# Performance work log

Hardware: AMD Instinct MI355X
Metric: run time of the kernel (lower is better)

## Reference

```python
import jax, jax.numpy as jnp
import numpy as np
import math

B, S, D, H = 2, 2048, 1024, 16
HD = D // H
KL_GAMMA = 0.1
EPS = 1e-10


def setup_inputs() -> dict:
    key = jax.random.key(0)
    ks = jax.random.split(key, 12)
    # positive inputs + positive weights keep scores > 0 so log(mean(scores)) is finite
    query = jax.random.uniform(ks[0], (B, S, D), dtype=jnp.float32)
    k_in = jax.random.uniform(ks[1], (B, S, D), dtype=jnp.float32)
    v_in = jax.random.uniform(ks[2], (B, S, D), dtype=jnp.float32)
    def w(k):
        return jax.random.uniform(k, (D, D), dtype=jnp.float32) * 0.002
    b = jnp.full((D,), 1e-3, dtype=jnp.float32)
    return {
        "query": query, "key": k_in, "value": v_in,
        "Wq": w(ks[3]), "bq": b,
        "Wk": w(ks[4]), "bk": b,
        "Wv": w(ks[5]), "bv": b,
        "Wo": w(ks[6]), "bo": b,
    }


def reference(query, key, value, Wq, bq, Wk, bk, Wv, bv, Wo, bo):
    Bq, Sq, _ = query.shape
    Sk = key.shape[1]
    # projections, split heads: [B, H, S, HD]
    Q = (query @ Wq + bq).reshape(Bq, Sq, H, HD).transpose(0, 2, 1, 3)
    K = (key @ Wk + bk).reshape(Bq, Sk, H, HD).transpose(0, 2, 1, 3)
    V = (value @ Wv + bv).reshape(Bq, Sk, H, HD).transpose(0, 2, 1, 3)
    scores = jnp.einsum("bhqd,bhkd->bhqk", Q, K) / math.sqrt(HD)  # [B,H,Sq,Sk]
    # KL bias: row-mean broadcast over keys, then log
    target = jnp.mean(scores, axis=-1, keepdims=True)  # [B,H,Sq,1]
    scores = scores + KL_GAMMA * jnp.log(target + EPS)
    attn = jax.nn.softmax(scores, axis=-1)
    ctx = jnp.einsum("bhqk,bhkd->bhqd", attn, V)
    ctx = ctx.transpose(0, 2, 1, 3).reshape(Bq, Sq, D)
    return ctx @ Wo + bo
```

## Files before the change

### kernel.cpp

```cpp
#include <hip/hip_runtime.h>
#include <hip/hip_bf16.h>
#include <stdint.h>


#define NB 2
#define NS 2048
#define ND 1024
#define NH 16
#define HD 64

typedef short bf16x8 __attribute__((ext_vector_type(8)));
typedef short bf16x4 __attribute__((ext_vector_type(4)));
typedef float f32x4 __attribute__((ext_vector_type(4)));
typedef float f32x16 __attribute__((ext_vector_type(16)));
typedef unsigned int u32x4 __attribute__((ext_vector_type(4)));

static __device__ __forceinline__ short f2bf(float f) {
    uint32_t u = __builtin_bit_cast(uint32_t, f);
    uint32_t r = (u + 0x7fffu + ((u >> 16) & 1u)) >> 16;
    return (short)(uint16_t)r;
}

static __device__ __forceinline__ unsigned int cvtpk(float lo, float hi) {
    unsigned int r;
    asm("v_cvt_pk_bf16_f32 %0, %1, %2" : "=v"(r) : "v"(lo), "v"(hi));
    return r;
}

#if __has_builtin(__builtin_amdgcn_exp2f)
#define EXP2(x) __builtin_amdgcn_exp2f(x)
#else
#define EXP2(x) exp2f(x)
#endif

static __device__ __forceinline__ void plswap(unsigned& a, unsigned& b) {
#if __has_builtin(__builtin_amdgcn_permlane32_swap)
    auto r = __builtin_amdgcn_permlane32_swap(a, b, false, false);
    a = r[0]; b = r[1];
#else
    const int l = (int)(threadIdx.x & 63);
    unsigned bl = __shfl(b, l & 31);
    unsigned ah = __shfl(a, (l & 31) + 32);
    a = (l < 32) ? a : bl;
    b = (l < 32) ? ah : b;
#endif
}

typedef __attribute__((address_space(1))) const unsigned int glob_u32;
typedef __attribute__((address_space(3))) unsigned int lds_u32;
static __device__ __forceinline__ void gload16(const void* g, void* l) {
    __builtin_amdgcn_global_load_lds((glob_u32*)g, (lds_u32*)l, 16, 0, 0);
}

__global__ __launch_bounds__(256) void prep_cast(const float* __restrict__ q,
                                                 const float* __restrict__ k,
                                                 const float* __restrict__ v,
                                                 short* __restrict__ Qo,
                                                 short* __restrict__ Ko,
                                                 short* __restrict__ Vo) {
    const float* src = (blockIdx.z == 0) ? q : (blockIdx.z == 1) ? k : v;
    short* dst = (blockIdx.z == 0) ? Qo : (blockIdx.z == 1) ? Ko : Vo;
    const size_t i = ((size_t)blockIdx.x * 256 + threadIdx.x) * 8;
    f32x4 a = *(const f32x4*)(src + i);
    f32x4 b = *(const f32x4*)(src + i + 4);
    bf16x8 o;
    o[0] = f2bf(a[0]); o[1] = f2bf(a[1]); o[2] = f2bf(a[2]); o[3] = f2bf(a[3]);
    o[4] = f2bf(b[0]); o[5] = f2bf(b[1]); o[6] = f2bf(b[2]); o[7] = f2bf(b[3]);
    *(bf16x8*)(dst + i) = o;
}

__global__ __launch_bounds__(256) void prep_wt(const float* __restrict__ W0,
                                               const float* __restrict__ W1,
                                               const float* __restrict__ W2,
                                               const float* __restrict__ W3,
                                               short* __restrict__ WtAll) {
    __shared__ short tile[32][33];
    const float* W = (blockIdx.z == 0) ? W0 : (blockIdx.z == 1) ? W1
                   : (blockIdx.z == 2) ? W2 : W3;
    short* Wt = WtAll + (size_t)blockIdx.z * (ND * ND);
    const int tx = threadIdx.x & 31;
    const int ty = threadIdx.x >> 5;
    const int k0 = blockIdx.x * 32, n0 = blockIdx.y * 32;
#pragma unroll
    for (int i = 0; i < 4; i++)
        tile[ty + i * 8][tx] = f2bf(W[(size_t)(k0 + ty + i * 8) * ND + n0 + tx]);
    __syncthreads();
#pragma unroll
    for (int i = 0; i < 4; i++)
        Wt[(size_t)(n0 + ty + i * 8) * ND + k0 + tx] = tile[tx][ty + i * 8];
}

static __device__ __forceinline__ void gemm_body(const short* __restrict__ A,
                                                 const short* __restrict__ Wt,
                                                 const float* __restrict__ bias,
                                                 void* __restrict__ Out,
                                                 int mode, float scale,
                                                 char* As2, char* Bs2) {
    const int tid = threadIdx.x;
    const int gm = blockIdx.x * 128;
    const int gn = blockIdx.y * 128;
    const int w = tid >> 6;
    const int l = tid & 63;
    const int r = l & 15;
    const int g = l >> 4;
    const int wr = w >> 1, wc = w & 1;

    f32x4 acc[4][4];
#pragma unroll
    for (int m = 0; m < 4; m++)
#pragma unroll
        for (int n = 0; n < 4; n++) acc[m][n] = (f32x4){0.f, 0.f, 0.f, 0.f};

    const int lin = ((w * 2) << 10) + l * 16;
#pragma unroll
    for (int j = 0; j < 2; j++) {
        const int lj = lin + (j << 10);
        const int row = lj >> 6;
        const int colL = (lj & 63) ^ (((row ^ (row >> 2)) & 3) << 4);
        gload16((const char*)A + (size_t)(gm + row) * (ND * 2) + colL, As2 + lj);
        gload16((const char*)Wt + (size_t)(gn + row) * (ND * 2) + colL, Bs2 + lj);
    }
    __syncthreads();

    for (int t = 0; t < ND / 32; t++) {
        const int cur = (t & 1) << 13;
        const int nxt = cur ^ 8192;
        if (t < ND / 32 - 1) {
            const int k0b = (t + 1) * 64;
#pragma unroll
            for (int j = 0; j < 2; j++) {
                const int lj = lin + (j << 10);
                const int row = lj >> 6;
                const int colL = (lj & 63) ^ (((row ^ (row >> 2)) & 3) << 4);
                gload16((const char*)A + (size_t)(gm + row) * (ND * 2) + k0b + colL,
                        As2 + nxt + lj);
                gload16((const char*)Wt + (size_t)(gn + row) * (ND * 2) + k0b + colL,
                        Bs2 + nxt + lj);
            }
        }

        bf16x8 af[4], bfv[4];
#pragma unroll
        for (int m = 0; m < 4; m++) {
            const int ar = wr * 64 + m * 16 + r;
            const int fa = ((ar ^ (ar >> 2)) & 3) << 4;
            af[m] = *(const bf16x8*)(As2 + cur + ar * 64 + ((g << 4) ^ fa));
        }
#pragma unroll
        for (int n = 0; n < 4; n++) {
            const int br = wc * 64 + n * 16 + r;
            const int fb = ((br ^ (br >> 2)) & 3) << 4;
            bfv[n] = *(const bf16x8*)(Bs2 + cur + br * 64 + ((g << 4) ^ fb));
        }
#pragma unroll
        for (int m = 0; m < 4; m++)
#pragma unroll
            for (int n = 0; n < 4; n++)
                acc[m][n] = __builtin_amdgcn_mfma_f32_16x16x32_bf16(
                    af[m], bfv[n], acc[m][n], 0, 0, 0);
        __syncthreads();
    }

#pragma unroll
    for (int m = 0; m < 4; m++) {
        const int orow = gm + wr * 64 + m * 16 + g * 4;
#pragma unroll
        for (int n = 0; n < 4; n++) {
            const int ocol = gn + wc * 64 + n * 16 + r;
            const float bv = bias[ocol];
#pragma unroll
            for (int i = 0; i < 4; i++) {
                const float vout = (acc[m][n][i] + bv) * scale;
                const int row = orow + i;
                if (mode == 0) {
                    const int b = row >> 11, s = row & 2047;
                    const int h = ocol >> 6, hd = ocol & 63;
                    ((short*)Out)[(((size_t)(b * NH + h) * NS + s) << 6) + hd] = f2bf(vout);
                } else if (mode == 1) {
                    const int b = row >> 11, s = row & 2047;
                    const int h = ocol >> 6, hd = ocol & 63;
                    ((short*)Out)[((size_t)(b * NH + h) * HD + hd) * NS + s] = f2bf(vout);
                } else {
                    ((float*)Out)[(size_t)row * ND + ocol] = vout;
                }
            }
        }
    }
}

#define QSCALE 0.18033688011112042f

__global__ __launch_bounds__(256, 3) void gemm_qkv(const short* __restrict__ Qin,
                                                   const short* __restrict__ Kin,
                                                   const short* __restrict__ Vin,
                                                   const short* __restrict__ WtAll,
                                                   const float* __restrict__ bq,
                                                   const float* __restrict__ bk,
                                                   const float* __restrict__ bv,
                                                   short* __restrict__ Qo,
                                                   short* __restrict__ Ko,
                                                   short* __restrict__ Vto) {
    __shared__ __align__(16) char As[2 * 8192];
    __shared__ __align__(16) char Bs[2 * 8192];
    const int z = blockIdx.z;
    const short* A = (z == 0) ? Qin : (z == 1) ? Kin : Vin;
    const short* Wt = WtAll + (size_t)z * ND * ND;
    const float* bias = (z == 0) ? bq : (z == 1) ? bk : bv;
    void* Out = (z == 0) ? (void*)Qo : (z == 1) ? (void*)Ko : (void*)Vto;
    const float scale = (z == 0) ? QSCALE : 1.0f;
    const int mode = (z == 2) ? 1 : 0;
    gemm_body(A, Wt, bias, Out, mode, scale, As, Bs);
}

__global__ __launch_bounds__(256, 3) void gemm_fin(const short* __restrict__ Ctx,
                                                   const short* __restrict__ Wt,
                                                   const float* __restrict__ bo,
                                                   float* __restrict__ Out) {
    __shared__ __align__(16) char As[2 * 8192];
    __shared__ __align__(16) char Bs[2 * 8192];
    gemm_body(Ctx, Wt, bo, Out, 2, 1.0f, As, Bs);
}

static __device__ __forceinline__ void stage2(const char* Kp8, const char* Vp8,
                                              char* Kbuf, char* Vbuf,
                                              int t, int w, int l) {
#pragma unroll
    for (int jj = 0; jj < 2; jj++) {
        const int chunk = w * 2 + jj;
        const int half = chunk >> 3;
        const int lin = ((chunk & 7) << 10) + l * 16;
        const int sw = lin ^ (((lin >> 7) & 7) << 4);
        const int row = sw >> 7, col = sw & 127;
        gload16(Kp8 + (size_t)(half * 1024 + t * 64 + row) * 128 + col,
                Kbuf + half * 8192 + ((chunk & 7) << 10));
        gload16(Vp8 + (size_t)row * (NS * 2) + (half * 1024 + t * 64) * 2 + col,
                Vbuf + half * 8192 + ((chunk & 7) << 10));
    }
}

__global__ __launch_bounds__(512, 4) void attn_kern(const short* __restrict__ Q,
                                                    const short* __restrict__ K,
                                                    const short* __restrict__ Vt,
                                                    short* __restrict__ Ctx) {
    __shared__ __align__(16) char smem[2][2][16384];

    const int tid = threadIdx.x;
    const int w = tid >> 6;
    const int l = tid & 63;
    const int c = l & 31;
    const int h = l >> 5;
    const int h16 = h << 4;

    const int bid = blockIdx.x;
    const int swb = (bid & 7) * 64 + (bid >> 3);
    const int bh = swb >> 4;
    const int qt = swb & 15;
    const int qb = qt * 128 + (w & 3) * 32;

    const short* Qp = Q + (size_t)bh * NS * HD;
    const char* Kp8 = (const char*)(K + (size_t)bh * NS * HD);
    const char* Vp8 = (const char*)(Vt + (size_t)bh * HD * NS);

    bf16x8 qf[4];
    {
        const short* Qrow = Qp + (size_t)(qb + c) * HD;
#pragma unroll
        for (int st = 0; st < 4; st++)
            qf[st] = *(const bf16x8*)(Qrow + st * 16 + h * 8);
    }

    f32x16 acc[2];
    acc[0] = (f32x16)(0.f);
    acc[1] = (f32x16)(0.f);
    float rsum = 0.f;

    const int khalf = w >> 2;
    const int sx = (c & 7) << 4;

    stage2(Kp8, Vp8, smem[0][0], smem[0][1], 0, w, l);
    __syncthreads();

    int bufi = 0;
    for (int t = 0; t < 16; t++) {
        if (t < 15)
            stage2(Kp8, Vp8, smem[bufi ^ 1][0], smem[bufi ^ 1][1], t + 1, w, l);

        const char* Kt = smem[bufi][0] + khalf * 8192;
        const char* Vv = smem[bufi][1] + khalf * 8192;

#pragma unroll
        for (int ktile = 0; ktile < 2; ktile++) {
            bf16x8 kf[4];
#pragma unroll
            for (int st = 0; st < 4; st++)
                kf[st] = *(const bf16x8*)(Kt + ((ktile * 32 + c) << 7) +
                                          ((st * 32 + h16) ^ sx));
            f32x16 S = (f32x16)(0.f);
#pragma unroll
            for (int st = 0; st < 4; st++)
                S = __builtin_amdgcn_mfma_f32_32x32x16_bf16(kf[st], qf[st], S, 0, 0, 0);

            float tv[16];
#pragma unroll
            for (int i = 0; i < 16; i++) { tv[i] = EXP2(S[i]); rsum += tv[i]; }

            unsigned v0[4], v1[4];
#pragma unroll
            for (int q4 = 0; q4 < 4; q4++) {
                v0[q4] = cvtpk(tv[4 * q4], tv[4 * q4 + 1]);
                v1[q4] = cvtpk(tv[4 * q4 + 2], tv[4 * q4 + 3]);
            }

#pragma unroll
            for (int ks = 0; ks < 2; ks++) {
                unsigned a0 = v0[2 * ks], b0 = v0[2 * ks + 1];
                unsigned a1 = v1[2 * ks], b1 = v1[2 * ks + 1];
                plswap(a0, b0);
                plswap(a1, b1);
                u32x4 paw; paw[0] = a0; paw[1] = a1; paw[2] = b0; paw[3] = b1;
                bf16x8 pa = __builtin_bit_cast(bf16x8, paw);
#pragma unroll
                for (int dt = 0; dt < 2; dt++) {
                    bf16x8 vb = *(const bf16x8*)(Vv + ((dt * 32 + c) << 7) +
                                                 ((ktile * 64 + ks * 32 + h16) ^ sx));
                    acc[dt] = __builtin_amdgcn_mfma_f32_32x32x16_bf16(pa, vb, acc[dt], 0, 0, 0);
                }
            }
        }
        __syncthreads();
        bufi ^= 1;
    }

    rsum += __shfl_xor(rsum, 32);

    float* rsbuf = (float*)&smem[0][0][0];
    float* sumbuf = (float*)&smem[0][0][0] + 256;
    if (h == 0) rsbuf[w * 32 + c] = rsum;
    if (w >= 4) {
#pragma unroll
        for (int q4 = 0; q4 < 4; q4++)
#pragma unroll
            for (int i = 0; i < 4; i++) {
                const int qrow = i + 8 * q4 + 4 * h;
#pragma unroll
                for (int dt = 0; dt < 2; dt++)
                    sumbuf[(((w - 4) * 32 + qrow) << 6) + dt * 32 + c] = acc[dt][q4 * 4 + i];
            }
    }
    __syncthreads();
    if (w < 4) {
        const int b = bh >> 4, hh = bh & 15;
#pragma unroll
        for (int q4 = 0; q4 < 4; q4++)
#pragma unroll
            for (int i = 0; i < 4; i++) {
                const int qrow = i + 8 * q4 + 4 * h;
                const float inv = 1.0f / (rsbuf[w * 32 + qrow] + rsbuf[(w + 4) * 32 + qrow]);
                short* op = Ctx + ((size_t)b * NS + qb + qrow) * ND + hh * HD;
#pragma unroll
                for (int dt = 0; dt < 2; dt++) {
                    const float vsum = acc[dt][q4 * 4 + i] +
                                       sumbuf[((w * 32 + qrow) << 6) + dt * 32 + c];
                    op[dt * 32 + c] = f2bf(vsum * inv);
                }
            }
    }
}

extern "C" void kernel_launch(void* const* d_in, const int* in_sizes, int n_in,
                              void* d_out, int out_size, void* d_ws, size_t ws_size,
                              hipStream_t stream) {
    (void)in_sizes; (void)n_in; (void)out_size; (void)ws_size;
    const float* query = (const float*)d_in[0];
    const float* key_  = (const float*)d_in[1];
    const float* value = (const float*)d_in[2];
    const float* Wq = (const float*)d_in[3];
    const float* bq = (const float*)d_in[4];
    const float* Wk = (const float*)d_in[5];
    const float* bk = (const float*)d_in[6];
    const float* Wv = (const float*)d_in[7];
    const float* bv = (const float*)d_in[8];
    const float* Wo = (const float*)d_in[9];
    const float* bo = (const float*)d_in[10];

    char* ws = (char*)d_ws;
    const size_t MB = 1024 * 1024;
    short* WtAll = (short*)ws;
    short* Qin = (short*)(ws + 8 * MB);
    short* Kin = (short*)(ws + 16 * MB);
    short* Vin = (short*)(ws + 24 * MB);
    short* Qb  = (short*)(ws + 32 * MB);
    short* Kb  = (short*)(ws + 40 * MB);
    short* Vtb = (short*)(ws + 48 * MB);
    short* Ctx = (short*)(ws + 8 * MB);

    prep_cast<<<dim3(2048, 1, 3), 256, 0, stream>>>(query, key_, value, Qin, Kin, Vin);
    prep_wt<<<dim3(32, 32, 4), 256, 0, stream>>>(Wq, Wk, Wv, Wo, WtAll);
    gemm_qkv<<<dim3(32, 8, 3), 256, 0, stream>>>(Qin, Kin, Vin, WtAll, bq, bk, bv,
                                                 Qb, Kb, Vtb);
    attn_kern<<<dim3(512), 512, 0, stream>>>(Qb, Kb, Vtb, Ctx);
    gemm_fin<<<dim3(32, 8), 256, 0, stream>>>(Ctx, WtAll + 3 * ND * ND, bo, (float*)d_out);
}
```

Baseline: 119.1 us.

## Replace QKV projection GEMM with 256x256-tile pipelined MFMA kernel

Replaces the 128x128-tile QKV projection GEMM with a 512-thread kernel using 256x256 output tiles, 64-wide K steps and double-buffered 64KB LDS stages with XOR swizzle. Global-to-LDS loads for the next stage are interleaved into four MFMA phases with explicit vmcnt waits, barriers and priority hints to overlap memory and compute. The change aims for higher operand reuse and fewer LDS/global loads per FLOP. In exchange the grid shrinks to 192 blocks, which may under-fill the GPU's CUs, and the output GEMM helper is simplified to the fp32 path only.

```diff
diff --git a/kernel.cpp b/kernel.cpp
--- a/kernel.cpp
+++ b/kernel.cpp
@@ -51,6 +51,9 @@
 static __device__ __forceinline__ void gload16(const void* g, void* l) {
     __builtin_amdgcn_global_load_lds((glob_u32*)g, (lds_u32*)l, 16, 0, 0);
 }
+
+#define VMW(N) do { asm volatile("s_waitcnt vmcnt(" #N ")" ::: "memory"); \
+                    __builtin_amdgcn_sched_barrier(0); } while (0)
 
 __global__ __launch_bounds__(256) void prep_cast(const float* __restrict__ q,
                                                  const float* __restrict__ k,
@@ -90,11 +93,130 @@
         Wt[(size_t)(n0 + ty + i * 8) * ND + k0 + tx] = tile[tx][ty + i * 8];
 }
 
+#define QSCALE 0.18033688011112042f
+
+#define QPHASE(mh, ks, S1, S2, WAIT)                                          \
+  {                                                                           \
+    bf16x8 af[4], bfr[4];                                                     \
+    _Pragma("unroll") for (int i = 0; i < 4; i++) {                           \
+      const int arow = wm * 128 + ((mh) * 4 + i) * 16 + r;                    \
+      af[i] = *(const bf16x8*)(ldsA + arow * 128 +                            \
+               ((((ks) * 64) + g * 16) ^ ((arow & 7) << 4)));                 \
+      const int brow = wn * 64 + i * 16 + r;                                  \
+      bfr[i] = *(const bf16x8*)(ldsB + brow * 128 +                           \
+               ((((ks) * 64) + g * 16) ^ ((brow & 7) << 4)));                 \
+    }                                                                         \
+    S1; S2;                                                                   \
+    __builtin_amdgcn_s_setprio(1);                                            \
+    _Pragma("unroll") for (int m = 0; m < 4; m++)                             \
+      _Pragma("unroll") for (int n = 0; n < 4; n++)                           \
+        acc[(mh) * 4 + m][n] = __builtin_amdgcn_mfma_f32_16x16x32_bf16(       \
+            af[m], bfr[n], acc[(mh) * 4 + m][n], 0, 0, 0);                    \
+    __builtin_amdgcn_s_setprio(0);                                            \
+    WAIT;                                                                     \
+    __builtin_amdgcn_s_barrier();                                             \
+    __builtin_amdgcn_sched_barrier(0);                                        \
+  }
+
+__global__ __launch_bounds__(512, 2) void gemm_qkv256(
+    const short* __restrict__ Qin, const short* __restrict__ Kin,
+    const short* __restrict__ Vin, const short* __restrict__ WtAll,
+    const float* __restrict__ bq, const float* __restrict__ bk,
+    const float* __restrict__ bv,
+    short* __restrict__ Qo, short* __restrict__ Ko, short* __restrict__ Vto) {
+    __shared__ __align__(16) char lds[2][65536];
+
+    const int z = blockIdx.z;
+    const short* Ain = (z == 0) ? Qin : (z == 1) ? Kin : Vin;
+    const char* Ap = (const char*)Ain;
+    const char* Wp = (const char*)(WtAll + (size_t)z * ND * ND);
+    const float* bias = (z == 0) ? bq : (z == 1) ? bk : bv;
+    const float scale = (z == 0) ? QSCALE : 1.0f;
+    const int mode = (z == 2) ? 1 : 0;
+    void* Out = (z == 0) ? (void*)Qo : (z == 1) ? (void*)Ko : (void*)Vto;
+
+    const int tid = threadIdx.x;
+    const int w = tid >> 6, l = tid & 63, r = l & 15, g = l >> 4;
+    const int wm = w >> 2, wn = w & 3;
+    const int gm = blockIdx.x * 256, gn = blockIdx.y * 256;
+
+    const int lin = tid * 16;
+    const int rowc = lin >> 7, colc = lin & 127;
+    const int colg = colc ^ ((rowc & 7) << 4);
+
+    const char* srcB[4];
+    const char* srcA[4];
+#pragma unroll
+    for (int c = 0; c < 4; c++)
+        srcB[c] = Wp + (size_t)(gn + c * 64 + rowc) * 2048 + colg;
+#pragma unroll
+    for (int q = 0; q < 4; q++)
+        srcA[q] = Ap + (size_t)(gm + q * 64 + rowc) * 2048 + colg;
+
+    auto STAGE = [&](int buf, int isA, int c, int tt) {
+        const char* src = (isA ? srcA[c] : srcB[c]) + tt * 128;
+        char* dst = (char*)lds[buf] + (isA ? 0 : 32768) + c * 8192 + lin;
+        gload16(src, dst);
+    };
+
+    f32x4 acc[8][4];
+#pragma unroll
+    for (int m = 0; m < 8; m++)
+#pragma unroll
+        for (int n = 0; n < 4; n++) acc[m][n] = (f32x4){0.f, 0.f, 0.f, 0.f};
+
+#pragma unroll
+    for (int c = 0; c < 4; c++) STAGE(0, 0, c, 0);
+#pragma unroll
+    for (int q = 0; q < 4; q++) STAGE(0, 1, q, 0);
+    asm volatile("s_waitcnt vmcnt(0)" ::: "memory");
+    __builtin_amdgcn_s_barrier();
+    __builtin_amdgcn_sched_barrier(0);
+
+    for (int t = 0; t < 15; t++) {
+        const int b = t & 1, nb = b ^ 1;
+        const char* ldsA = lds[b];
+        const char* ldsB = lds[b] + 32768;
+        QPHASE(0, 0, STAGE(nb, 0, 0, t + 1), STAGE(nb, 0, 1, t + 1), ((void)0));
+        QPHASE(0, 1, STAGE(nb, 0, 2, t + 1), STAGE(nb, 0, 3, t + 1), VMW(4));
+        QPHASE(1, 0, STAGE(nb, 1, 0, t + 1), STAGE(nb, 1, 2, t + 1), ((void)0));
+        QPHASE(1, 1, STAGE(nb, 1, 1, t + 1), STAGE(nb, 1, 3, t + 1), VMW(2));
+    }
+    {
+        const char* ldsA = lds[1];
+        const char* ldsB = lds[1] + 32768;
+        QPHASE(0, 0, ((void)0), ((void)0), ((void)0));
+        QPHASE(0, 1, ((void)0), ((void)0), ((void)0));
+        QPHASE(1, 0, ((void)0), ((void)0), ((void)0));
+        QPHASE(1, 1, ((void)0), ((void)0), ((void)0));
+    }
+
+#pragma unroll
+    for (int mf = 0; mf < 8; mf++) {
+        const int orow0 = gm + wm * 128 + mf * 16 + g * 4;
+#pragma unroll
+        for (int n = 0; n < 4; n++) {
+            const int ocol = gn + wn * 64 + n * 16 + r;
+            const float bvv = bias[ocol];
+#pragma unroll
+            for (int i = 0; i < 4; i++) {
+                const float vout = (acc[mf][n][i] + bvv) * scale;
+                const int row = orow0 + i;
+                const int bb = row >> 11, s = row & 2047;
+                const int h = ocol >> 6, hd = ocol & 63;
+                if (mode == 0)
+                    ((short*)Out)[(((size_t)(bb * NH + h) * NS + s) << 6) + hd] = f2bf(vout);
+                else
+                    ((short*)Out)[((size_t)(bb * NH + h) * HD + hd) * NS + s] = f2bf(vout);
+            }
+        }
+    }
+}
+
 static __device__ __forceinline__ void gemm_body(const short* __restrict__ A,
                                                  const short* __restrict__ Wt,
                                                  const float* __restrict__ bias,
-                                                 void* __restrict__ Out,
-                                                 int mode, float scale,
+                                                 float* __restrict__ Out,
                                                  char* As2, char* Bs2) {
     const int tid = threadIdx.x;
     const int gm = blockIdx.x * 128;
@@ -138,7 +260,6 @@
                         Bs2 + nxt + lj);
             }
         }
-
         bf16x8 af[4], bfv[4];
 #pragma unroll
         for (int m = 0; m < 4; m++) {
@@ -169,47 +290,10 @@
             const int ocol = gn + wc * 64 + n * 16 + r;
             const float bv = bias[ocol];
 #pragma unroll
-            for (int i = 0; i < 4; i++) {
-                const float vout = (acc[m][n][i] + bv) * scale;
-                const int row = orow + i;
-                if (mode == 0) {
-                    const int b = row >> 11, s = row & 2047;
-                    const int h = ocol >> 6, hd = ocol & 63;
-                    ((short*)Out)[(((size_t)(b * NH + h) * NS + s) << 6) + hd] = f2bf(vout);
-                } else if (mode == 1) {
-                    const int b = row >> 11, s = row & 2047;
-                    const int h = ocol >> 6, hd = ocol & 63;
-                    ((short*)Out)[((size_t)(b * NH + h) * HD + hd) * NS + s] = f2bf(vout);
-                } else {
-                    ((float*)Out)[(size_t)row * ND + ocol] = vout;
-                }
-            }
-        }
-    }
-}
-
-#define QSCALE 0.18033688011112042f
-
-__global__ __launch_bounds__(256, 3) void gemm_qkv(const short* __restrict__ Qin,
-                                                   const short* __restrict__ Kin,
-                                                   const short* __restrict__ Vin,
-                                                   const short* __restrict__ WtAll,
-                                                   const float* __restrict__ bq,
-                                                   const float* __restrict__ bk,
-                                                   const float* __restrict__ bv,
-                                                   short* __restrict__ Qo,
-                                                   short* __restrict__ Ko,
-                                                   short* __restrict__ Vto) {
-    __shared__ __align__(16) char As[2 * 8192];
-    __shared__ __align__(16) char Bs[2 * 8192];
-    const int z = blockIdx.z;
-    const short* A = (z == 0) ? Qin : (z == 1) ? Kin : Vin;
-    const short* Wt = WtAll + (size_t)z * ND * ND;
-    const float* bias = (z == 0) ? bq : (z == 1) ? bk : bv;
-    void* Out = (z == 0) ? (void*)Qo : (z == 1) ? (void*)Ko : (void*)Vto;
-    const float scale = (z == 0) ? QSCALE : 1.0f;
-    const int mode = (z == 2) ? 1 : 0;
-    gemm_body(A, Wt, bias, Out, mode, scale, As, Bs);
+            for (int i = 0; i < 4; i++)
+                Out[(size_t)(orow + i) * ND + ocol] = acc[m][n][i] + bv;
+        }
+    }
 }
 
 __global__ __launch_bounds__(256, 3) void gemm_fin(const short* __restrict__ Ctx,
@@ -218,7 +302,7 @@
                                                    float* __restrict__ Out) {
     __shared__ __align__(16) char As[2 * 8192];
     __shared__ __align__(16) char Bs[2 * 8192];
-    gemm_body(Ctx, Wt, bo, Out, 2, 1.0f, As, Bs);
+    gemm_body(Ctx, Wt, bo, Out, As, Bs);
 }
 
 static __device__ __forceinline__ void stage2(const char* Kp8, const char* Vp8,
@@ -396,8 +480,8 @@
 
     prep_cast<<<dim3(2048, 1, 3), 256, 0, stream>>>(query, key_, value, Qin, Kin, Vin);
     prep_wt<<<dim3(32, 32, 4), 256, 0, stream>>>(Wq, Wk, Wv, Wo, WtAll);
-    gemm_qkv<<<dim3(32, 8, 3), 256, 0, stream>>>(Qin, Kin, Vin, WtAll, bq, bk, bv,
-                                                 Qb, Kb, Vtb);
+    gemm_qkv256<<<dim3(16, 4, 3), 512, 0, stream>>>(Qin, Kin, Vin, WtAll, bq, bk, bv,
+                                                    Qb, Kb, Vtb);
     attn_kern<<<dim3(512), 512, 0, stream>>>(Qb, Kb, Vtb, Ctx);
     gemm_fin<<<dim3(32, 8), 256, 0, stream>>>(Ctx, WtAll + 3 * ND * ND, bo, (float*)d_out);
 }
```

Measured after the change: 133.8 us. 1.12x slower.

## Process two query tiles per warp in attention to reuse K/V tiles

Applied to the files above, without the earlier changes.

Each warp now computes 64 query rows (two 32-row MFMA tiles) against each staged K/V tile, doubling reuse of shared-memory K and V loads and halving the grid to 256 blocks. Row sums move to a dedicated shared buffer and the cross-half reduction is extended to cover both query chunks. This raises register pressure (launch bounds relaxed to 2 blocks/CU) and leaves only one block per CU, reducing latency hiding.

```diff
diff --git a/kernel.cpp b/kernel.cpp
--- a/kernel.cpp
+++ b/kernel.cpp
@@ -138,7 +138,6 @@
                         Bs2 + nxt + lj);
             }
         }
-
         bf16x8 af[4], bfv[4];
 #pragma unroll
         for (int m = 0; m < 4; m++) {
@@ -238,11 +237,12 @@
     }
 }
 
-__global__ __launch_bounds__(512, 4) void attn_kern(const short* __restrict__ Q,
+__global__ __launch_bounds__(512, 2) void attn_kern(const short* __restrict__ Q,
                                                     const short* __restrict__ K,
                                                     const short* __restrict__ Vt,
                                                     short* __restrict__ Ctx) {
     __shared__ __align__(16) char smem[2][2][16384];
+    __shared__ float rsbuf[8][2][32];
 
     const int tid = threadIdx.x;
     const int w = tid >> 6;
@@ -252,29 +252,32 @@
     const int h16 = h << 4;
 
     const int bid = blockIdx.x;
-    const int swb = (bid & 7) * 64 + (bid >> 3);
-    const int bh = swb >> 4;
-    const int qt = swb & 15;
-    const int qb = qt * 128 + (w & 3) * 32;
+    const int swb = (bid & 7) * 32 + (bid >> 3);
+    const int bh = swb >> 3;
+    const int qt = swb & 7;
+    const int g = w & 3;
+    const int khalf = w >> 2;
+    const int qw = qt * 256 + g * 64;
 
     const short* Qp = Q + (size_t)bh * NS * HD;
     const char* Kp8 = (const char*)(K + (size_t)bh * NS * HD);
     const char* Vp8 = (const char*)(Vt + (size_t)bh * HD * NS);
 
-    bf16x8 qf[4];
-    {
-        const short* Qrow = Qp + (size_t)(qb + c) * HD;
+    bf16x8 qf[2][4];
+#pragma unroll
+    for (int qc = 0; qc < 2; qc++)
 #pragma unroll
         for (int st = 0; st < 4; st++)
-            qf[st] = *(const bf16x8*)(Qrow + st * 16 + h * 8);
-    }
-
-    f32x16 acc[2];
-    acc[0] = (f32x16)(0.f);
-    acc[1] = (f32x16)(0.f);
-    float rsum = 0.f;
-
-    const int khalf = w >> 2;
+            qf[qc][st] = *(const bf16x8*)(Qp + (size_t)(qw + qc * 32 + c) * HD +
+                                          st * 16 + h * 8);
+
+    f32x16 acc[2][2];
+#pragma unroll
+    for (int qc = 0; qc < 2; qc++)
+#pragma unroll
+        for (int dt = 0; dt < 2; dt++) acc[qc][dt] = (f32x16)(0.f);
+    float rs0 = 0.f, rs1 = 0.f;
+
     const int sx = (c & 7) << 4;
 
     stage2(Kp8, Vp8, smem[0][0], smem[0][1], 0, w, l);
@@ -295,35 +298,46 @@
             for (int st = 0; st < 4; st++)
                 kf[st] = *(const bf16x8*)(Kt + ((ktile * 32 + c) << 7) +
                                           ((st * 32 + h16) ^ sx));
-            f32x16 S = (f32x16)(0.f);
-#pragma unroll
-            for (int st = 0; st < 4; st++)
-                S = __builtin_amdgcn_mfma_f32_32x32x16_bf16(kf[st], qf[st], S, 0, 0, 0);
-
-            float tv[16];
-#pragma unroll
-            for (int i = 0; i < 16; i++) { tv[i] = EXP2(S[i]); rsum += tv[i]; }
-
-            unsigned v0[4], v1[4];
+            f32x16 S0 = (f32x16)(0.f), S1 = (f32x16)(0.f);
+#pragma unroll
+            for (int st = 0; st < 4; st++) {
+                S0 = __builtin_amdgcn_mfma_f32_32x32x16_bf16(kf[st], qf[0][st], S0, 0, 0, 0);
+                S1 = __builtin_amdgcn_mfma_f32_32x32x16_bf16(kf[st], qf[1][st], S1, 0, 0, 0);
+            }
+
+            float tv0[16], tv1[16];
+#pragma unroll
+            for (int i = 0; i < 16; i++) {
+                tv0[i] = EXP2(S0[i]); rs0 += tv0[i];
+                tv1[i] = EXP2(S1[i]); rs1 += tv1[i];
+            }
+            unsigned p0a[4], p0b[4], p1a[4], p1b[4];
 #pragma unroll
             for (int q4 = 0; q4 < 4; q4++) {
-                v0[q4] = cvtpk(tv[4 * q4], tv[4 * q4 + 1]);
-                v1[q4] = cvtpk(tv[4 * q4 + 2], tv[4 * q4 + 3]);
+                p0a[q4] = cvtpk(tv0[4 * q4], tv0[4 * q4 + 1]);
+                p0b[q4] = cvtpk(tv0[4 * q4 + 2], tv0[4 * q4 + 3]);
+                p1a[q4] = cvtpk(tv1[4 * q4], tv1[4 * q4 + 1]);
+                p1b[q4] = cvtpk(tv1[4 * q4 + 2], tv1[4 * q4 + 3]);
             }
 
 #pragma unroll
             for (int ks = 0; ks < 2; ks++) {
-                unsigned a0 = v0[2 * ks], b0 = v0[2 * ks + 1];
-                unsigned a1 = v1[2 * ks], b1 = v1[2 * ks + 1];
-                plswap(a0, b0);
-                plswap(a1, b1);
-                u32x4 paw; paw[0] = a0; paw[1] = a1; paw[2] = b0; paw[3] = b1;
-                bf16x8 pa = __builtin_bit_cast(bf16x8, paw);
+                unsigned a0 = p0a[2 * ks], b0 = p0a[2 * ks + 1];
+                unsigned a1 = p0b[2 * ks], b1 = p0b[2 * ks + 1];
+                plswap(a0, b0); plswap(a1, b1);
+                u32x4 pw0; pw0[0] = a0; pw0[1] = a1; pw0[2] = b0; pw0[3] = b1;
+                bf16x8 pa0 = __builtin_bit_cast(bf16x8, pw0);
+                unsigned c0 = p1a[2 * ks], d0 = p1a[2 * ks + 1];
+                unsigned c1 = p1b[2 * ks], d1 = p1b[2 * ks + 1];
+                plswap(c0, d0); plswap(c1, d1);
+                u32x4 pw1; pw1[0] = c0; pw1[1] = c1; pw1[2] = d0; pw1[3] = d1;
+                bf16x8 pa1 = __builtin_bit_cast(bf16x8, pw1);
 #pragma unroll
                 for (int dt = 0; dt < 2; dt++) {
                     bf16x8 vb = *(const bf16x8*)(Vv + ((dt * 32 + c) << 7) +
                                                  ((ktile * 64 + ks * 32 + h16) ^ sx));
-                    acc[dt] = __builtin_amdgcn_mfma_f32_32x32x16_bf16(pa, vb, acc[dt], 0, 0, 0);
+                    acc[0][dt] = __builtin_amdgcn_mfma_f32_32x32x16_bf16(pa0, vb, acc[0][dt], 0, 0, 0);
+                    acc[1][dt] = __builtin_amdgcn_mfma_f32_32x32x16_bf16(pa1, vb, acc[1][dt], 0, 0, 0);
                 }
             }
         }
@@ -331,39 +345,47 @@
         bufi ^= 1;
     }
 
-    rsum += __shfl_xor(rsum, 32);
-
-    float* rsbuf = (float*)&smem[0][0][0];
-    float* sumbuf = (float*)&smem[0][0][0] + 256;
-    if (h == 0) rsbuf[w * 32 + c] = rsum;
+    rs0 += __shfl_xor(rs0, 32);
+    rs1 += __shfl_xor(rs1, 32);
+    if (h == 0) { rsbuf[w][0][c] = rs0; rsbuf[w][1][c] = rs1; }
+
+    float* sumbuf = (float*)&smem[0][0][0];
     if (w >= 4) {
 #pragma unroll
-        for (int q4 = 0; q4 < 4; q4++)
-#pragma unroll
-            for (int i = 0; i < 4; i++) {
-                const int qrow = i + 8 * q4 + 4 * h;
-#pragma unroll
-                for (int dt = 0; dt < 2; dt++)
-                    sumbuf[(((w - 4) * 32 + qrow) << 6) + dt * 32 + c] = acc[dt][q4 * 4 + i];
-            }
+        for (int qc = 0; qc < 2; qc++)
+#pragma unroll
+            for (int q4 = 0; q4 < 4; q4++)
+#pragma unroll
+                for (int i = 0; i < 4; i++) {
+                    const int qrow = qc * 32 + i + 8 * q4 + 4 * h;
+#pragma unroll
+                    for (int dt = 0; dt < 2; dt++)
+                        sumbuf[((g * 64 + qrow) << 6) + dt * 32 + c] =
+                            acc[qc][dt][q4 * 4 + i];
+                }
     }
     __syncthreads();
     if (w < 4) {
         const int b = bh >> 4, hh = bh & 15;
 #pragma unroll
-        for (int q4 = 0; q4 < 4; q4++)
-#pragma unroll
-            for (int i = 0; i < 4; i++) {
-                const int qrow = i + 8 * q4 + 4 * h;
-                const float inv = 1.0f / (rsbuf[w * 32 + qrow] + rsbuf[(w + 4) * 32 + qrow]);
-                short* op = Ctx + ((size_t)b * NS + qb + qrow) * ND + hh * HD;
-#pragma unroll
-                for (int dt = 0; dt < 2; dt++) {
-                    const float vsum = acc[dt][q4 * 4 + i] +
-                                       sumbuf[((w * 32 + qrow) << 6) + dt * 32 + c];
-                    op[dt * 32 + c] = f2bf(vsum * inv);
+        for (int qc = 0; qc < 2; qc++)
+#pragma unroll
+            for (int q4 = 0; q4 < 4; q4++)
+#pragma unroll
+                for (int i = 0; i < 4; i++) {
+                    const int qrow32 = i + 8 * q4 + 4 * h;
+                    const int qrow = qc * 32 + qrow32;
+                    const float inv = 1.0f / (rsbuf[g][qc][qrow32] +
+                                              rsbuf[4 + g][qc][qrow32]);
+                    short* op = Ctx + ((size_t)b * NS + qt * 256 + g * 64 + qrow) * ND +
+                                hh * HD;
+#pragma unroll
+                    for (int dt = 0; dt < 2; dt++) {
+                        const float val = acc[qc][dt][q4 * 4 + i] +
+                                          sumbuf[((g * 64 + qrow) << 6) + dt * 32 + c];
+                        op[dt * 32 + c] = f2bf(val * inv);
+                    }
                 }
-            }
     }
 }
 
@@ -398,6 +420,6 @@
     prep_wt<<<dim3(32, 32, 4), 256, 0, stream>>>(Wq, Wk, Wv, Wo, WtAll);
     gemm_qkv<<<dim3(32, 8, 3), 256, 0, stream>>>(Qin, Kin, Vin, WtAll, bq, bk, bv,
                                                  Qb, Kb, Vtb);
-    attn_kern<<<dim3(512), 512, 0, stream>>>(Qb, Kb, Vtb, Ctx);
+    attn_kern<<<dim3(256), 512, 0, stream>>>(Qb, Kb, Vtb, Ctx);
     gemm_fin<<<dim3(32, 8), 256, 0, stream>>>(Ctx, WtAll + 3 * ND * ND, bo, (float*)d_out);
 }
```

New measurement: 119.1 us. No clear change (+0.0%).
